# Kernel tuning notes

Measured on AMD Instinct MI355X. Metric: run time of the kernel, lower is better.

## Reference

```python
import jax, jax.numpy as jnp
import numpy as np

N = 100000      # nodes
E = 1600000     # directed edges (avg degree 16)
F_IN = 256      # in_feats
H = 4           # num_heads
D = 32          # n_hidden per head
NEG_SLOPE = 0.2


def setup_inputs() -> dict:
    key = jax.random.key(0)
    k_feat, k_src, k_dst, k_perm, k_w, k_a = jax.random.split(key, 6)
    features = jax.random.normal(k_feat, (N, F_IN), dtype=jnp.float32)
    src = jax.random.randint(k_src, (E,), 0, N, dtype=jnp.int32)
    dst = jax.random.randint(k_dst, (E,), 0, N, dtype=jnp.int32)
    # fixed instance of torch.randperm(N) for the corrupt=True gather
    perm = jax.random.permutation(k_perm, N).astype(jnp.int32)
    W = jax.random.normal(k_w, (F_IN, H * D), dtype=jnp.float32) / np.sqrt(F_IN)
    a = jax.random.normal(k_a, (2, H, D), dtype=jnp.float32) * 0.1
    return dict(features=features, W=W, attn_l=a[0], attn_r=a[1],
                src=src, dst=dst, perm=perm)


def reference(features, W, attn_l, attn_r, src, dst, perm):
    # corrupt=True path: node-permutation gather
    x = features[perm]                                  # [N, F_IN]
    # GAT layer: shared linear projection -> [N, H, D]
    h = (x @ W).reshape(N, H, D)
    # per-node attention half-scores
    el = jnp.sum(h * attn_l, axis=-1)                   # [N, H]
    er = jnp.sum(h * attn_r, axis=-1)                   # [N, H]
    # per-edge raw attention (gather)
    e = jax.nn.leaky_relu(el[src] + er[dst], NEG_SLOPE)  # [E, H]
    # softmax over edges grouped by destination node (segment softmax)
    emax = jax.ops.segment_max(e, dst, num_segments=N)  # [N, H]
    ee = jnp.exp(e - emax[dst])                         # [E, H]
    denom = jax.ops.segment_sum(ee, dst, num_segments=N)  # [N, H]
    alpha = ee / denom[dst]                             # [E, H]
    # weighted neighbor aggregation (gather-scale-scatter)
    msg = h[src] * alpha[:, :, None]                    # [E, H, D]
    out = jax.ops.segment_sum(msg, dst, num_segments=N)  # [N, H, D]
    return jax.nn.elu(out.reshape(N, H * D))            # [N, 128]
```

## Files before the change

kernel.cpp:

```cpp
#include <hip/hip_runtime.h>
#include <hip/hip_bf16.h>
#include <math.h>

#define N_NODES 100000
#define E_EDGES 1600000
#define F_IN    256
#define HD      128
#define NHEAD   4
#define DHEAD   32
#define NEG_SLOPE 0.2f
#define NBIN    200
#define BINW    500
#define CHUNK   8192
#define NCHUNK  196
#define BINCAP  16384
#define NC      144
#define NCT     9
#define GEMS1   196
#define GEMS2   195

typedef __attribute__((ext_vector_type(8))) __bf16 bf16x8;
typedef __attribute__((ext_vector_type(4))) float  f32x4;
typedef __attribute__((ext_vector_type(8))) unsigned short u16x8;

__device__ __forceinline__ unsigned short f2bf(float x) {
    unsigned int b = __float_as_uint(x);
    b += 0x7fffu + ((b >> 16) & 1u);
    return (unsigned short)(b >> 16);
}
__device__ __forceinline__ float bf2f(unsigned short u) {
    return __uint_as_float((unsigned int)u << 16);
}

__global__ void k_prep(const float* __restrict__ W, const float* __restrict__ al,
                       const float* __restrict__ ar, unsigned short* __restrict__ wbf,
                       int* __restrict__ cursor) {
    if (blockIdx.x == 0) {
        for (int i = threadIdx.x; i < NBIN; i += NC) cursor[i] = 0;
    }
    const int k = blockIdx.x;
    const int c = threadIdx.x;
    float v;
    if (c < 128) {
        v = W[k * HD + c];
    } else if (c < 132) {
        int h = c - 128; float s = 0.f;
        for (int d = 0; d < DHEAD; d++) s += W[k * HD + h * DHEAD + d] * al[h * DHEAD + d];
        v = s;
    } else if (c < 136) {
        int h = c - 132; float s = 0.f;
        for (int d = 0; d < DHEAD; d++) s += W[k * HD + h * DHEAD + d] * ar[h * DHEAD + d];
        v = s;
    } else {
        v = 0.f;
    }
    *(unsigned short*)((char*)wbf + (size_t)c * 512 + ((2 * k) ^ ((c & 7) << 4))) = f2bf(v);
}

__device__ __forceinline__ void gemm_role(int bid, int tid,
        unsigned char* smem, const float* __restrict__ X,
        const unsigned short* __restrict__ wbf, const int* __restrict__ perm,
        unsigned short* __restrict__ hb, float* __restrict__ el,
        float* __restrict__ er) {
    unsigned short* Bs = (unsigned short*)smem;
    {
        const float4* srcv = (const float4*)wbf;
        float4* dstv = (float4*)Bs;
#pragma unroll
        for (int i = 0; i < 9; i++) dstv[tid + i * 512] = srcv[tid + i * 512];
    }
    __syncthreads();

    const int l   = tid & 63;
    const int wv  = tid >> 6;
    const int l15 = l & 15;
    const int kg  = l >> 4;
    const int rowbase = bid * 256 + wv * 32;

    int r0 = rowbase + l15;      if (r0 >= N_NODES) r0 = N_NODES - 1;
    int r1 = rowbase + 16 + l15; if (r1 >= N_NODES) r1 = N_NODES - 1;
    const float* aptr0 = X + (long)perm[r0] * F_IN + kg * 8;
    const float* aptr1 = X + (long)perm[r1] * F_IN + kg * 8;

    f32x4 acc[2][NCT];
#pragma unroll
    for (int rt = 0; rt < 2; rt++)
#pragma unroll
        for (int ct = 0; ct < NCT; ct++) acc[rt][ct] = (f32x4){0.f, 0.f, 0.f, 0.f};

#pragma unroll
    for (int k0 = 0; k0 < F_IN; k0 += 32) {
        bf16x8 a0, a1;
        {
            float4 v0 = *(const float4*)(aptr0 + k0);
            float4 v1 = *(const float4*)(aptr0 + k0 + 4);
            a0[0]=(__bf16)v0.x; a0[1]=(__bf16)v0.y; a0[2]=(__bf16)v0.z; a0[3]=(__bf16)v0.w;
            a0[4]=(__bf16)v1.x; a0[5]=(__bf16)v1.y; a0[6]=(__bf16)v1.z; a0[7]=(__bf16)v1.w;
        }
        {
            float4 v0 = *(const float4*)(aptr1 + k0);
            float4 v1 = *(const float4*)(aptr1 + k0 + 4);
            a1[0]=(__bf16)v0.x; a1[1]=(__bf16)v0.y; a1[2]=(__bf16)v0.z; a1[3]=(__bf16)v0.w;
            a1[4]=(__bf16)v1.x; a1[5]=(__bf16)v1.y; a1[6]=(__bf16)v1.z; a1[7]=(__bf16)v1.w;
        }
        const int sb = k0 * 2 + kg * 16;
#pragma unroll
        for (int ct = 0; ct < NCT; ct++) {
            int c = ct * 16 + l15;
            bf16x8 b = *(const bf16x8*)((const char*)Bs + c * 512 + (sb ^ ((c & 7) << 4)));
            acc[0][ct] = __builtin_amdgcn_mfma_f32_16x16x32_bf16(a0, b, acc[0][ct], 0, 0, 0);
            acc[1][ct] = __builtin_amdgcn_mfma_f32_16x16x32_bf16(a1, b, acc[1][ct], 0, 0, 0);
        }
    }

#pragma unroll
    for (int rt = 0; rt < 2; rt++)
#pragma unroll
        for (int i = 0; i < 4; i++) {
            int row = rowbase + rt * 16 + kg * 4 + i;
            if (row < N_NODES) {
                unsigned short* op = hb + (long)row * HD + l15;
#pragma unroll
                for (int ct = 0; ct < 8; ct++) op[ct * 16] = f2bf(acc[rt][ct][i]);
                float v = acc[rt][8][i];
                if (l15 < 4)      el[(long)row * 4 + l15]       = v;
                else if (l15 < 8) er[(long)row * 4 + (l15 - 4)] = v;
            }
        }
}

__global__ __launch_bounds__(512, 4) void k_fat1(const float* __restrict__ X,
        const unsigned short* __restrict__ wbf, const int* __restrict__ perm,
        unsigned short* __restrict__ hb, float* __restrict__ el, float* __restrict__ er,
        const int* __restrict__ src, const int* __restrict__ dst,
        int* __restrict__ cursor, unsigned int* __restrict__ binbuf) {
    __shared__ __align__(16) unsigned char smem[73728];
    const int tid = threadIdx.x;

    if (blockIdx.x < NCHUNK) {
        unsigned int*  buf     = (unsigned int*)smem;
        unsigned char* binid   = smem + 32768;
        unsigned int*  hist    = (unsigned int*)(smem + 40960);
        unsigned int*  pfx     = (unsigned int*)(smem + 41792);
        unsigned int*  base_sh = (unsigned int*)(smem + 42624);
        unsigned int*  cnt2    = (unsigned int*)(smem + 43456);
        const int e0 = blockIdx.x * CHUNK;
        const int n = min(CHUNK, E_EDGES - e0);

        for (int i = tid; i < NBIN; i += 512) { hist[i] = 0; cnt2[i] = 0; }
        __syncthreads();
        for (int i = tid; i < n; i += 512) {
            int d = dst[e0 + i];
            atomicAdd(&hist[d / BINW], 1u);
        }
        __syncthreads();
        if (tid < NBIN) pfx[tid] = hist[tid];
        __syncthreads();
        for (int off = 1; off < NBIN; off <<= 1) {
            unsigned v = (tid < NBIN) ? pfx[tid] : 0;
            unsigned u = (tid >= off && tid < NBIN) ? pfx[tid - off] : 0;
            __syncthreads();
            if (tid < NBIN) pfx[tid] = v + u;
            __syncthreads();
        }
        if (tid < NBIN) base_sh[tid] = (unsigned)atomicAdd(cursor + tid, (int)hist[tid]);
        __syncthreads();
        for (int i = tid; i < n; i += 512) {
            int d = dst[e0 + i];
            int s = src[e0 + i];
            int b = d / BINW;
            unsigned pos = atomicAdd(&cnt2[b], 1u);
            unsigned idx = pfx[b] - hist[b] + pos;
            buf[idx] = ((unsigned)(d - b * BINW) << 17) | (unsigned)s;
            binid[idx] = (unsigned char)b;
        }
        __syncthreads();
        for (int i = tid; i < n; i += 512) {
            int b = binid[i];
            unsigned ex = pfx[b] - hist[b];
            unsigned gpos = base_sh[b] + ((unsigned)i - ex);
            if (gpos < BINCAP) binbuf[(long)b * BINCAP + gpos] = buf[i];
        }
    } else {
        gemm_role(blockIdx.x - NCHUNK, tid, smem, X, wbf, perm, hb, el, er);
    }
}

__global__ __launch_bounds__(512, 4) void k_fat2(const unsigned int* __restrict__ binbuf,
        const int* __restrict__ cursor, int* __restrict__ cnt, int* __restrict__ basearr,
        int* __restrict__ csr,
        const float* __restrict__ X, const unsigned short* __restrict__ wbf,
        const int* __restrict__ perm, unsigned short* __restrict__ hb,
        float* __restrict__ el, float* __restrict__ er) {
    __shared__ __align__(16) unsigned char smem[73728];
    const int tid = threadIdx.x;
    if (blockIdx.x < NBIN) {
        int* cnt_l = (int*)smem;
        int* pfx_l = (int*)(smem + 2048);
        int* pos_l = (int*)(smem + 4096);
        int* redsh = (int*)(smem + 6144);
        const int b = blockIdx.x;
        const int n = min(cursor[b], BINCAP);

        int part = (tid < b) ? min(cursor[tid], BINCAP) : 0;
#pragma unroll
        for (int off = 32; off; off >>= 1) part += __shfl_xor(part, off, 64);
        if ((tid & 63) == 0) redsh[tid >> 6] = part;
        for (int i = tid; i < BINW; i += 512) { cnt_l[i] = 0; pos_l[i] = 0; }
        __syncthreads();
        if (tid == 0) {
            int s = 0;
            for (int i = 0; i < 8; i++) s += redsh[i];
            redsh[8] = s;
        }
        __syncthreads();
        const int binbase = redsh[8];

        const unsigned int* bp = binbuf + (long)b * BINCAP;
        for (int i = tid; i < n; i += 512) atomicAdd(&cnt_l[bp[i] >> 17], 1);
        __syncthreads();
        if (tid < BINW) pfx_l[tid] = cnt_l[tid];
        __syncthreads();
        for (int off = 1; off < BINW; off <<= 1) {
            int v = (tid < BINW) ? pfx_l[tid] : 0;
            int u = (tid >= off && tid < BINW) ? pfx_l[tid - off] : 0;
            __syncthreads();
            if (tid < BINW) pfx_l[tid] = v + u;
            __syncthreads();
        }
        for (int i = tid; i < n; i += 512) {
            unsigned p = bp[i];
            int dl = (int)(p >> 17);
            int s  = (int)(p & 0x1FFFFu);
            int pos = atomicAdd(&pos_l[dl], 1);
            csr[binbase + (pfx_l[dl] - cnt_l[dl]) + pos] = s;
        }
        __syncthreads();
        for (int i = tid; i < BINW; i += 512) {
            int gd = b * BINW + i;
            cnt[gd]     = cnt_l[i];
            basearr[gd] = binbase + pfx_l[i] - cnt_l[i];
        }
    } else {
        gemm_role(GEMS1 + (blockIdx.x - NBIN), tid, smem, X, wbf, perm, hb, el, er);
    }
}

__global__ __launch_bounds__(256) void k_aggr(const float* __restrict__ el,
        const float* __restrict__ er, const int* __restrict__ cnt,
        const int* __restrict__ basearr, const int* __restrict__ csr,
        const unsigned short* __restrict__ hb, float* __restrict__ out) {
    int wid = (int)((blockIdx.x * (long)blockDim.x + threadIdx.x) >> 6);
    if (wid >= N_NODES) return;
    const int lane = threadIdx.x & 63;
    const int g    = lane >> 4;
    const int l4   = lane & 15;
    const int head = l4 >> 2;
    int deg = cnt[wid];
    if (deg > 64) deg = 64;
    const int base = basearr[wid];
    const float ern = er[(long)wid * 4 + head];
    int myS = (lane < deg) ? csr[base + lane] : 0;
    float acc[8];
#pragma unroll
    for (int j = 0; j < 8; j++) acc[j] = 0.f;
    float asum = 0.f;
    for (int i = 0; i < deg; i += 4) {
        int e = i + g;
        int s = __shfl(myS, e & 63, 64);
        u16x8 hv = *(const u16x8*)(hb + (long)s * HD + l4 * 8);
        float a = 0.f;
        if (e < deg) {
            float v = el[(long)s * 4 + head] + ern;
            v = v > 0.f ? v : NEG_SLOPE * v;
            a = __expf(v);
        }
        asum += a;
#pragma unroll
        for (int j = 0; j < 8; j++) acc[j] += bf2f(hv[j]) * a;
    }
#pragma unroll
    for (int off = 16; off <= 32; off <<= 1) {
        asum += __shfl_xor(asum, off, 64);
#pragma unroll
        for (int j = 0; j < 8; j++) acc[j] += __shfl_xor(acc[j], off, 64);
    }
    if (g == 0) {
        float inv = asum > 0.f ? 1.f / asum : 0.f;
        float4 o0, o1;
        float t;
        t = acc[0] * inv; o0.x = t > 0.f ? t : __expf(t) - 1.f;
        t = acc[1] * inv; o0.y = t > 0.f ? t : __expf(t) - 1.f;
        t = acc[2] * inv; o0.z = t > 0.f ? t : __expf(t) - 1.f;
        t = acc[3] * inv; o0.w = t > 0.f ? t : __expf(t) - 1.f;
        t = acc[4] * inv; o1.x = t > 0.f ? t : __expf(t) - 1.f;
        t = acc[5] * inv; o1.y = t > 0.f ? t : __expf(t) - 1.f;
        t = acc[6] * inv; o1.z = t > 0.f ? t : __expf(t) - 1.f;
        t = acc[7] * inv; o1.w = t > 0.f ? t : __expf(t) - 1.f;
        float* op = out + (long)wid * HD + l4 * 8;
        *(float4*)op = o0;
        *(float4*)(op + 4) = o1;
    }
}

extern "C" void kernel_launch(void* const* d_in, const int* in_sizes, int n_in,
                              void* d_out, int out_size, void* d_ws, size_t ws_size,
                              hipStream_t stream) {
    const float* features = (const float*)d_in[0];
    const float* W        = (const float*)d_in[1];
    const float* attn_l   = (const float*)d_in[2];
    const float* attn_r   = (const float*)d_in[3];
    const int*   src      = (const int*)d_in[4];
    const int*   dst      = (const int*)d_in[5];
    const int*   perm     = (const int*)d_in[6];
    float* out = (float*)d_out;

    char* ws = (char*)d_ws;
    const size_t OFF_HB   = 0;
    const size_t OFF_EL   = 25600000;
    const size_t OFF_ER   = 27200000;
    const size_t OFF_CNT  = 28800000;
    const size_t OFF_BASE = 29200000;
    const size_t OFF_CUR  = 29600000;
    const size_t OFF_WBF  = 29604096;
    const size_t OFF_CSR  = 29686016;
    const size_t OFF_BINB = 36086016;

    unsigned short* hb    = (unsigned short*)(ws + OFF_HB);
    float* el     = (float*)(ws + OFF_EL);
    float* er     = (float*)(ws + OFF_ER);
    int*   cnt    = (int*)(ws + OFF_CNT);
    int*   basearr= (int*)(ws + OFF_BASE);
    int*   cursor = (int*)(ws + OFF_CUR);
    unsigned short* wbf = (unsigned short*)(ws + OFF_WBF);
    int*   csr    = (int*)(ws + OFF_CSR);
    unsigned int* binbuf = (unsigned int*)(ws + OFF_BINB);

    k_prep<<<F_IN, NC, 0, stream>>>(W, attn_l, attn_r, wbf, cursor);
    k_fat1<<<NCHUNK + GEMS1, 512, 0, stream>>>(features, wbf, perm, hb, el, er,
                                               src, dst, cursor, binbuf);
    k_fat2<<<NBIN + GEMS2, 512, 0, stream>>>(binbuf, cursor, cnt, basearr, csr,
                                             features, wbf, perm, hb, el, er);
    k_aggr<<<(N_NODES * 64 + 255) / 256, 256, 0, stream>>>(el, er, cnt, basearr, csr,
                                                           hb, out);
}
```

Baseline: 130.4 us.

## Store features in column-slice-major layout and split aggregation by feature slice

The GEMM epilogue now writes h as eight 16-column slices, each stored contiguously for all nodes, and writes el/er head-major. The aggregation kernel gives each block one slice (blockIdx & 7) and a group of 32 nodes, with each wave looping over 8 nodes and 8 edges per iteration. The aim is a smaller gather working set per slice so it stays in cache, since blocks with neighbouring indices touch the same slice. In exchange, CSR indices, degrees and er are reloaded once per slice (8x), each gather is only 4 bytes per lane, and the GEMM epilogue stores become more scattered.

```diff
diff --git a/kernel.cpp b/kernel.cpp
--- a/kernel.cpp
+++ b/kernel.cpp
@@ -21,7 +21,6 @@
 
 typedef __attribute__((ext_vector_type(8))) __bf16 bf16x8;
 typedef __attribute__((ext_vector_type(4))) float  f32x4;
-typedef __attribute__((ext_vector_type(8))) unsigned short u16x8;
 
 __device__ __forceinline__ unsigned short f2bf(float x) {
     unsigned int b = __float_as_uint(x);
@@ -60,7 +59,7 @@
 __device__ __forceinline__ void gemm_role(int bid, int tid,
         unsigned char* smem, const float* __restrict__ X,
         const unsigned short* __restrict__ wbf, const int* __restrict__ perm,
-        unsigned short* __restrict__ hb, float* __restrict__ el,
+        unsigned short* __restrict__ hbt, float* __restrict__ el,
         float* __restrict__ er) {
     unsigned short* Bs = (unsigned short*)smem;
     {
@@ -119,19 +118,19 @@
         for (int i = 0; i < 4; i++) {
             int row = rowbase + rt * 16 + kg * 4 + i;
             if (row < N_NODES) {
-                unsigned short* op = hb + (long)row * HD + l15;
-#pragma unroll
-                for (int ct = 0; ct < 8; ct++) op[ct * 16] = f2bf(acc[rt][ct][i]);
+#pragma unroll
+                for (int ct = 0; ct < 8; ct++)
+                    hbt[((long)ct * N_NODES + row) * 16 + l15] = f2bf(acc[rt][ct][i]);
                 float v = acc[rt][8][i];
-                if (l15 < 4)      el[(long)row * 4 + l15]       = v;
-                else if (l15 < 8) er[(long)row * 4 + (l15 - 4)] = v;
+                if (l15 < 4)      el[(long)l15 * N_NODES + row]       = v;
+                else if (l15 < 8) er[(long)(l15 - 4) * N_NODES + row] = v;
             }
         }
 }
 
 __global__ __launch_bounds__(512, 4) void k_fat1(const float* __restrict__ X,
         const unsigned short* __restrict__ wbf, const int* __restrict__ perm,
-        unsigned short* __restrict__ hb, float* __restrict__ el, float* __restrict__ er,
+        unsigned short* __restrict__ hbt, float* __restrict__ el, float* __restrict__ er,
         const int* __restrict__ src, const int* __restrict__ dst,
         int* __restrict__ cursor, unsigned int* __restrict__ binbuf) {
     __shared__ __align__(16) unsigned char smem[73728];
@@ -182,7 +181,7 @@
             if (gpos < BINCAP) binbuf[(long)b * BINCAP + gpos] = buf[i];
         }
     } else {
-        gemm_role(blockIdx.x - NCHUNK, tid, smem, X, wbf, perm, hb, el, er);
+        gemm_role(blockIdx.x - NCHUNK, tid, smem, X, wbf, perm, hbt, el, er);
     }
 }
 
@@ -190,7 +189,7 @@
         const int* __restrict__ cursor, int* __restrict__ cnt, int* __restrict__ basearr,
         int* __restrict__ csr,
         const float* __restrict__ X, const unsigned short* __restrict__ wbf,
-        const int* __restrict__ perm, unsigned short* __restrict__ hb,
+        const int* __restrict__ perm, unsigned short* __restrict__ hbt,
         float* __restrict__ el, float* __restrict__ er) {
     __shared__ __align__(16) unsigned char smem[73728];
     const int tid = threadIdx.x;
@@ -242,64 +241,61 @@
             basearr[gd] = binbase + pfx_l[i] - cnt_l[i];
         }
     } else {
-        gemm_role(GEMS1 + (blockIdx.x - NBIN), tid, smem, X, wbf, perm, hb, el, er);
+        gemm_role(GEMS1 + (blockIdx.x - NBIN), tid, smem, X, wbf, perm, hbt, el, er);
     }
 }
 
 __global__ __launch_bounds__(256) void k_aggr(const float* __restrict__ el,
         const float* __restrict__ er, const int* __restrict__ cnt,
         const int* __restrict__ basearr, const int* __restrict__ csr,
-        const unsigned short* __restrict__ hb, float* __restrict__ out) {
-    int wid = (int)((blockIdx.x * (long)blockDim.x + threadIdx.x) >> 6);
-    if (wid >= N_NODES) return;
-    const int lane = threadIdx.x & 63;
-    const int g    = lane >> 4;
-    const int l4   = lane & 15;
-    const int head = l4 >> 2;
-    int deg = cnt[wid];
-    if (deg > 64) deg = 64;
-    const int base = basearr[wid];
-    const float ern = er[(long)wid * 4 + head];
-    int myS = (lane < deg) ? csr[base + lane] : 0;
-    float acc[8];
-#pragma unroll
-    for (int j = 0; j < 8; j++) acc[j] = 0.f;
-    float asum = 0.f;
-    for (int i = 0; i < deg; i += 4) {
-        int e = i + g;
-        int s = __shfl(myS, e & 63, 64);
-        u16x8 hv = *(const u16x8*)(hb + (long)s * HD + l4 * 8);
-        float a = 0.f;
-        if (e < deg) {
-            float v = el[(long)s * 4 + head] + ern;
-            v = v > 0.f ? v : NEG_SLOPE * v;
-            a = __expf(v);
-        }
-        asum += a;
-#pragma unroll
-        for (int j = 0; j < 8; j++) acc[j] += bf2f(hv[j]) * a;
-    }
-#pragma unroll
-    for (int off = 16; off <= 32; off <<= 1) {
-        asum += __shfl_xor(asum, off, 64);
-#pragma unroll
-        for (int j = 0; j < 8; j++) acc[j] += __shfl_xor(acc[j], off, 64);
-    }
-    if (g == 0) {
-        float inv = asum > 0.f ? 1.f / asum : 0.f;
-        float4 o0, o1;
-        float t;
-        t = acc[0] * inv; o0.x = t > 0.f ? t : __expf(t) - 1.f;
-        t = acc[1] * inv; o0.y = t > 0.f ? t : __expf(t) - 1.f;
-        t = acc[2] * inv; o0.z = t > 0.f ? t : __expf(t) - 1.f;
-        t = acc[3] * inv; o0.w = t > 0.f ? t : __expf(t) - 1.f;
-        t = acc[4] * inv; o1.x = t > 0.f ? t : __expf(t) - 1.f;
-        t = acc[5] * inv; o1.y = t > 0.f ? t : __expf(t) - 1.f;
-        t = acc[6] * inv; o1.z = t > 0.f ? t : __expf(t) - 1.f;
-        t = acc[7] * inv; o1.w = t > 0.f ? t : __expf(t) - 1.f;
-        float* op = out + (long)wid * HD + l4 * 8;
-        *(float4*)op = o0;
-        *(float4*)(op + 4) = o1;
+        const unsigned short* __restrict__ hbt, float* __restrict__ out) {
+    const int slice = blockIdx.x & 7;
+    const int nb    = blockIdx.x >> 3;
+    const int wv    = threadIdx.x >> 6;
+    const int lane  = threadIdx.x & 63;
+    const int g     = lane >> 3;
+    const int l3    = lane & 7;
+    const int head  = slice >> 1;
+    const unsigned short* hs = hbt + (long)slice * N_NODES * 16;
+    const float* elh = el + (long)head * N_NODES;
+    const float* erh = er + (long)head * N_NODES;
+
+    const int node0 = nb * 32 + wv * 8;
+#pragma unroll 1
+    for (int nn = 0; nn < 8; nn++) {
+        const int node = node0 + nn;
+        int deg = cnt[node];
+        if (deg > 64) deg = 64;
+        const int base = basearr[node];
+        const float ern = erh[node];
+        int myS = (lane < deg) ? csr[base + lane] : 0;
+        float a0 = 0.f, a1 = 0.f, asum = 0.f;
+        for (int i = 0; i < deg; i += 8) {
+            int e = i + g;
+            int s = __shfl(myS, e & 63, 64);
+            ushort2 hv = *(const ushort2*)(hs + (long)s * 16 + l3 * 2);
+            float a = 0.f;
+            if (e < deg) {
+                float v = elh[s] + ern;
+                v = v > 0.f ? v : NEG_SLOPE * v;
+                a = __expf(v);
+            }
+            asum += a;
+            a0 += bf2f(hv.x) * a;
+            a1 += bf2f(hv.y) * a;
+        }
+#pragma unroll
+        for (int off = 8; off <= 32; off <<= 1) {
+            asum += __shfl_xor(asum, off, 64);
+            a0 += __shfl_xor(a0, off, 64);
+            a1 += __shfl_xor(a1, off, 64);
+        }
+        if (g == 0) {
+            float inv = asum > 0.f ? 1.f / asum : 0.f;
+            float t0 = a0 * inv; t0 = t0 > 0.f ? t0 : __expf(t0) - 1.f;
+            float t1 = a1 * inv; t1 = t1 > 0.f ? t1 : __expf(t1) - 1.f;
+            *(float2*)(out + (long)node * HD + slice * 16 + l3 * 2) = make_float2(t0, t1);
+        }
     }
 }
 
@@ -316,7 +312,7 @@
     float* out = (float*)d_out;
 
     char* ws = (char*)d_ws;
-    const size_t OFF_HB   = 0;
+    const size_t OFF_HBT  = 0;
     const size_t OFF_EL   = 25600000;
     const size_t OFF_ER   = 27200000;
     const size_t OFF_CNT  = 28800000;
@@ -326,7 +322,7 @@
     const size_t OFF_CSR  = 29686016;
     const size_t OFF_BINB = 36086016;
 
-    unsigned short* hb    = (unsigned short*)(ws + OFF_HB);
+    unsigned short* hbt   = (unsigned short*)(ws + OFF_HBT);
     float* el     = (float*)(ws + OFF_EL);
     float* er     = (float*)(ws + OFF_ER);
     int*   cnt    = (int*)(ws + OFF_CNT);
@@ -337,10 +333,9 @@
     unsigned int* binbuf = (unsigned int*)(ws + OFF_BINB);
 
     k_prep<<<F_IN, NC, 0, stream>>>(W, attn_l, attn_r, wbf, cursor);
-    k_fat1<<<NCHUNK + GEMS1, 512, 0, stream>>>(features, wbf, perm, hb, el, er,
+    k_fat1<<<NCHUNK + GEMS1, 512, 0, stream>>>(features, wbf, perm, hbt, el, er,
                                                src, dst, cursor, binbuf);
     k_fat2<<<NBIN + GEMS2, 512, 0, stream>>>(binbuf, cursor, cnt, basearr, csr,
-                                             features, wbf, perm, hb, el, er);
-    k_aggr<<<(N_NODES * 64 + 255) / 256, 256, 0, stream>>>(el, er, cnt, basearr, csr,
-                                                           hb, out);
-}
+                                             features, wbf, perm, hbt, el, er);
+    k_aggr<<<8 * (N_NODES / 32), 256, 0, stream>>>(el, er, cnt, basearr, csr, hbt, out);
+}
```

After: 267.0 us. +104.8%, slower.
